# Kernel tuning notes

Hardware: AMD Instinct MI355X
Metric: run time of the kernel (lower is better)

The kernel has to match this reference:

```python
import jax, jax.numpy as jnp
import numpy as np

N, IN_C, HID, OUT_C = 4096, 512, 512, 40
E = 131072
N_CLUSTERS, PCA_K, KMEANS_ITERS = 7, 10, 10
EPS = 1e-12


def _linear_params(key, fin, fout):
    k1, k2 = jax.random.split(key)
    lim = 1.0 / np.sqrt(fin)
    W = jax.random.uniform(k1, (fin, fout), jnp.float32, -lim, lim)
    b = jax.random.uniform(k2, (fout,), jnp.float32, -lim, lim)
    return W, b


def setup_inputs() -> dict:
    key = jax.random.key(0)
    ks = jax.random.split(key, 8)
    x = jax.random.normal(ks[0], (N, IN_C), jnp.float32)
    edge_index = jax.random.randint(ks[1], (2, E), 0, N, dtype=jnp.int32)
    y = jax.random.randint(ks[2], (N,), 0, N_CLUSTERS, dtype=jnp.int32)
    W_ego, b_ego = _linear_params(ks[3], IN_C, HID)
    W_cos, b_cos = _linear_params(ks[4], IN_C, HID)
    W_glob, b_glob = _linear_params(ks[5], IN_C, HID)
    W_fc, b_fc = _linear_params(ks[6], HID + IN_C + HID + HID, OUT_C)
    return dict(x=x, W_ego=W_ego, b_ego=b_ego, W_cos=W_cos, b_cos=b_cos,
                W_glob=W_glob, b_glob=b_glob, W_fc=W_fc, b_fc=b_fc,
                edge_index=edge_index, y=y)


def _mp_layer(x, W, b, src, dst):
    # MessagePassingLayer: scatter-add lin(x)[src] at dst, then relu
    h = x @ W + b
    agg = jax.ops.segment_sum(h[src], dst, num_segments=N)
    return jax.nn.relu(agg)


def _dominant_mask(x):
    # Dominant branch: PCA(10) -> KMeans(n_clusters) -> keep nodes with dist <= median.
    # sklearn's randomized KMeans replaced by deterministic Lloyd iterations
    # (init = first N_CLUSTERS rows); whole pipeline is detached in the original.
    xs = jax.lax.stop_gradient(x)
    xc = xs - xs.mean(0, keepdims=True)
    _, _, vt = jnp.linalg.svd(xc, full_matrices=False)
    feats = xc @ vt[:PCA_K].T  # [N, PCA_K]

    def step(c, _):
        d2 = ((feats[:, None, :] - c[None]) ** 2).sum(-1)  # [N, K]
        lab = jnp.argmin(d2, axis=1)
        sums = jax.ops.segment_sum(feats, lab, num_segments=N_CLUSTERS)
        cnt = jax.ops.segment_sum(jnp.ones((N,), jnp.float32), lab, num_segments=N_CLUSTERS)
        newc = jnp.where(cnt[:, None] > 0, sums / jnp.maximum(cnt, 1.0)[:, None], c)
        return newc, None

    centers, _ = jax.lax.scan(step, feats[:N_CLUSTERS], None, length=KMEANS_ITERS)
    d2 = ((feats[:, None, :] - centers[None]) ** 2).sum(-1)
    lab = jnp.argmin(d2, axis=1)
    dist = jnp.linalg.norm(feats - centers[lab], axis=1)
    keep = dist <= jnp.median(dist)
    return jax.lax.stop_gradient(keep.astype(jnp.float32))


def _forward(x, W_ego, b_ego, W_cos, b_cos, W_glob, b_glob, W_fc, b_fc, src, dst):
    # --- ego branch: exact 2-hop (source_to_target) subgraph mean per node ---
    # B[i, j] = 1 iff edge j->i; subset(i) = {i} | 1-hop | 2-hop (set semantics via >0)
    B = jnp.zeros((N, N), jnp.float32).at[dst, src].add(1.0)
    reach = jnp.eye(N, dtype=jnp.float32) + B + B @ B
    Mf = (reach > 0).astype(jnp.float32)
    ego_feats = (Mf @ x) / Mf.sum(1, keepdims=True)

    # --- Dominant branch: zero out far-from-center nodes ---
    keep = _dominant_mask(x)
    cut_enc = x * keep[:, None]

    # --- cosine branch: segment softmax over outgoing edges grouped by src ---
    norm_x = x / jnp.maximum(jnp.linalg.norm(x, axis=1, keepdims=True), EPS)
    sims = (norm_x[src] * norm_x[dst]).sum(-1)  # [E]
    smax = jax.ops.segment_max(sims, src, num_segments=N)
    ex = jnp.exp(sims - smax[src])
    den = jax.ops.segment_sum(ex, src, num_segments=N)
    w = ex / jnp.maximum(den, EPS)[src]
    num = jax.ops.segment_sum(w[:, None] * x[dst], src, num_segments=N)
    wsum = jax.ops.segment_sum(w, src, num_segments=N)
    deg = jax.ops.segment_sum(jnp.ones((E,), jnp.float32), src, num_segments=N)
    cos_feats = jnp.where(deg[:, None] > 0, num / jnp.maximum(wsum, EPS)[:, None], x)

    # --- encoders + head ---
    global_feats = x @ W_glob + b_glob
    ego_enc = _mp_layer(ego_feats, W_ego, b_ego, src, dst)
    cosine_enc = _mp_layer(cos_feats, W_cos, b_cos, src, dst)
    combined = jnp.concatenate([ego_enc, cut_enc, cosine_enc, global_feats], axis=-1)
    return jax.nn.log_softmax(combined @ W_fc + b_fc, axis=1)


def reference(x, W_ego, b_ego, W_cos, b_cos, W_glob, b_glob, W_fc, b_fc, edge_index, y):
    src, dst = edge_index[0], edge_index[1]
    return _forward(x, W_ego, b_ego, W_cos, b_cos, W_glob, b_glob, W_fc, b_fc, src, dst)
```

## Files before the change

### kernel.cpp

```cpp
#include <hip/hip_runtime.h>
#include <math.h>

#define NN 4096
#define NC 512
#define NE 131072
#define KM_BLOCKS 16

typedef __bf16 bf16x8 __attribute__((ext_vector_type(8)));
typedef float f32x4 __attribute__((ext_vector_type(4)));
typedef unsigned short u16x8 __attribute__((ext_vector_type(8)));

__device__ __forceinline__ unsigned short f2b(float f){
  unsigned u = __float_as_uint(f);
  u += 0x7fffu + ((u >> 16) & 1u);
  return (unsigned short)(u >> 16);
}
__device__ __forceinline__ float b2f(unsigned short h){
  return __uint_as_float(((unsigned)h) << 16);
}
__device__ __forceinline__ float wredsum(float v){
  #pragma unroll
  for (int o = 32; o; o >>= 1) v += __shfl_xor(v, o, 64);
  return v;
}
__device__ __forceinline__ float wredmax(float v){
  #pragma unroll
  for (int o = 32; o; o >>= 1) v = fmaxf(v, __shfl_xor(v, o, 64));
  return v;
}

__global__ __launch_bounds__(256) void k_transconv(const float* __restrict__ src, int R, int C,
    unsigned short* __restrict__ dstT, int ldT, unsigned short* __restrict__ dstD){
  __shared__ unsigned short tile[64][65];
  int bc = blockIdx.x * 64, br = blockIdx.y * 64;
  int t = threadIdx.x, lc = t & 63, lr4 = t >> 6;
  for (int j = 0; j < 16; ++j){
    int r = br + lr4*16 + j, c = bc + lc;
    float v = (r < R && c < C) ? src[(size_t)r*C + c] : 0.f;
    unsigned short b = f2b(v);
    tile[lr4*16+j][lc] = b;
    if (dstD && r < R && c < C) dstD[(size_t)r*C + c] = b;
  }
  __syncthreads();
  for (int j = 0; j < 16; ++j){
    int cc = bc + lr4*16 + j, rr = br + lc;
    if (cc < C && rr < R) dstT[(size_t)cc*ldT + rr] = tile[lc][lr4*16+j];
  }
}

__global__ __launch_bounds__(256) void k_normx(const float* __restrict__ x, unsigned short* __restrict__ nx){
  int wid = threadIdx.x >> 6, lane = threadIdx.x & 63;
  int row = blockIdx.x*4 + wid;
  const float* xr = x + (size_t)row*NC + lane*8;
  float v[8]; float ss = 0.f;
  #pragma unroll
  for (int j=0;j<8;j++){ v[j] = xr[j]; ss += v[j]*v[j]; }
  ss = wredsum(ss);
  float sc = 1.0f / fmaxf(sqrtf(ss), 1e-12f);
  u16x8 o;
  #pragma unroll
  for (int j=0;j<8;j++) o[j] = f2b(v[j]*sc);
  *(u16x8*)(nx + (size_t)row*NC + lane*8) = o;
}

__global__ void k_count_b1(const int* __restrict__ src, const int* __restrict__ dst,
    int* cin, int* cout, unsigned long long* B1){
  int e = blockIdx.x*256 + threadIdx.x;
  if (e < NE){
    int s = src[e], d = dst[e];
    atomicAdd(&cout[s], 1);
    atomicAdd(&cin[d], 1);
    atomicOr(&B1[(size_t)d*64 + (s>>6)], 1ull << (s & 63));
  }
}
__global__ __launch_bounds__(1024) void k_scan(const int* __restrict__ cnt0, const int* __restrict__ cnt1,
    int* off0, int* off1, int* fill0, int* fill1){
  __shared__ int s[1024];
  int t = threadIdx.x;
  for (int arr = 0; arr < 2; ++arr){
    const int* cnt = arr ? cnt1 : cnt0;
    int* off = arr ? off1 : off0;
    int* fill = arr ? fill1 : fill0;
    int a0 = cnt[t*4], a1 = cnt[t*4+1], a2 = cnt[t*4+2], a3 = cnt[t*4+3];
    int ts = a0+a1+a2+a3;
    s[t] = ts; __syncthreads();
    for (int o = 1; o < 1024; o <<= 1){
      int v = (t >= o) ? s[t-o] : 0; __syncthreads();
      s[t] += v; __syncthreads();
    }
    int ex = s[t] - ts;
    off[t*4] = ex; off[t*4+1] = ex+a0; off[t*4+2] = ex+a0+a1; off[t*4+3] = ex+a0+a1+a2;
    fill[t*4] = ex; fill[t*4+1] = ex+a0; fill[t*4+2] = ex+a0+a1; fill[t*4+3] = ex+a0+a1+a2;
    if (t == 1023) off[4096] = s[1023];
    __syncthreads();
  }
}
__global__ void k_fill(const int* __restrict__ src, const int* __restrict__ dst,
    int* fin, int* fout, int* csr_in, int* csr_out){
  int e = blockIdx.x*256 + threadIdx.x;
// ... 103 lines not shown

__global__ __launch_bounds__(256) void k_cos(const unsigned short* __restrict__ nx,
    const unsigned short* __restrict__ xb,
    const int* __restrict__ off_out, const int* __restrict__ csr_out,
    unsigned short* __restrict__ cosf){
  __shared__ float simsb[4][256];
  int wid = threadIdx.x >> 6, lane = threadIdx.x & 63;
  int node = blockIdx.x*4 + wid;
  float own[8];
  { u16x8 o = *(const u16x8*)(nx + (size_t)node*NC + lane*8);
    #pragma unroll
    for (int j=0;j<8;j++) own[j] = b2f(o[j]); }
  int beg = off_out[node], end = off_out[node+1], deg = end - beg;
  float m = -3.0e38f;
  for (int e = 0; e < deg; ++e){
    int d = csr_out[beg+e];
    u16x8 nb = *(const u16x8*)(nx + (size_t)d*NC + lane*8);
    float sp = 0.f;
    #pragma unroll
    for (int j=0;j<8;j++) sp += own[j]*b2f(nb[j]);
    float s = wredsum(sp);
    if (e < 256 && lane == 0) simsb[wid][e] = s;
    m = fmaxf(m, s);
  }
  float den = 0.f, acc[8] = {0,0,0,0,0,0,0,0};
  for (int e = 0; e < deg; ++e){
    int d = csr_out[beg+e];
    float s;
    if (e < 256) s = simsb[wid][e];
    else {
      u16x8 nb = *(const u16x8*)(nx + (size_t)d*NC + lane*8);
      float sp = 0.f;
      #pragma unroll
      for (int j=0;j<8;j++) sp += own[j]*b2f(nb[j]);
      s = wredsum(sp);
    }
    float w = expf(s - m);
    den += w;
    u16x8 xv = *(const u16x8*)(xb + (size_t)d*NC + lane*8);
    #pragma unroll
    for (int j=0;j<8;j++) acc[j] += w * b2f(xv[j]);
  }
  u16x8 o;
  if (deg > 0){
    float r = 1.0f/den;
    #pragma unroll
    for (int j=0;j<8;j++) o[j] = f2b(acc[j]*r);
  } else {
    o = *(const u16x8*)(xb + (size_t)node*NC + lane*8);
  }
  *(u16x8*)(cosf + (size_t)node*NC + lane*8) = o;
}

__global__ __launch_bounds__(256) void k_agg(const unsigned short* __restrict__ he,
    const unsigned short* __restrict__ hc,
    const int* __restrict__ off_in, const int* __restrict__ csr_in,
    unsigned short* __restrict__ comb){
  int wid = threadIdx.x >> 6, lane = threadIdx.x & 63;
  int node = blockIdx.x*4 + wid;
  float ae[8] = {0,0,0,0,0,0,0,0}, ac[8] = {0,0,0,0,0,0,0,0};
  int beg = off_in[node], end = off_in[node+1];
  for (int e = beg; e < end; ++e){
    int j = csr_in[e];
    u16x8 ve = *(const u16x8*)(he + (size_t)j*NC + lane*8);
    u16x8 vc = *(const u16x8*)(hc + (size_t)j*NC + lane*8);
    #pragma unroll
    for (int k=0;k<8;k++){ ae[k] += b2f(ve[k]); ac[k] += b2f(vc[k]); }
  }
  u16x8 oe, oc;
  #pragma unroll
  for (int k=0;k<8;k++){ oe[k] = f2b(fmaxf(ae[k], 0.f)); oc[k] = f2b(fmaxf(ac[k], 0.f)); }
  *(u16x8*)(comb + (size_t)node*2048 + lane*8) = oe;
  *(u16x8*)(comb + (size_t)node*2048 + 1024 + lane*8) = oc;
}

__global__ void k_cut(const unsigned short* __restrict__ xb, const float* __restrict__ keep,
    unsigned short* __restrict__ comb){
  int id = blockIdx.x*256 + threadIdx.x;
  int node = id >> 6, lane = id & 63;
  u16x8 xv = *(const u16x8*)(xb + (size_t)node*NC + lane*8);
  if (keep[node] == 0.f){
    #pragma unroll
    for (int j=0;j<8;j++) xv[j] = 0;
  }
  *(u16x8*)(comb + (size_t)node*2048 + 512 + lane*8) = xv;
}

__global__ __launch_bounds__(256) void k_lsm(const float* __restrict__ logits, float* __restrict__ out){
  int wid = threadIdx.x >> 6, lane = threadIdx.x & 63;
  int row = blockIdx.x*4 + wid;
  float v = (lane < 40) ? logits[(size_t)row*64 + lane] : -3.0e38f;
  float m = wredmax(v);
  float e = (lane < 40) ? expf(v - m) : 0.f;
  float s = wredsum(e);
  float l = logf(s);
  if (lane < 40) out[(size_t)row*40 + lane] = v - m - l;
}

__global__ void k_colmean(const float* __restrict__ x, double* __restrict__ meanbuf){
  int c0 = threadIdx.x;
  int r0 = blockIdx.x*128;
  double s0 = 0, s1 = 0;
  for (int r = r0; r < r0+128; ++r){
    s0 += (double)x[(size_t)r*NC + c0];
    s1 += (double)x[(size_t)r*NC + c0 + 256];
  }
  atomicAdd(&meanbuf[c0], s0);
  atomicAdd(&meanbuf[c0+256], s1);
}

__global__ __launch_bounds__(256) void k_cov(const float* __restrict__ x,
    const double* __restrict__ meanbuf, double* __restrict__ Cm){
  __shared__ float sa[16][33];
  __shared__ float sb[16][33];
  const int t = threadIdx.x;
  const int ti = t & 15, tj = t >> 4;
  const int bi = blockIdx.x, bj = blockIdx.y;
  int l0 = t, l1 = t + 256;
  int r0a = l0 >> 5, c0a = l0 & 31;
  int r1a = l1 >> 5, c1a = l1 & 31;
  float ma0 = (float)(meanbuf[bi*32 + c0a] * (1.0/4096.0));
  float ma1 = (float)(meanbuf[bi*32 + c1a] * (1.0/4096.0));
  float mb0 = (float)(meanbuf[bj*32 + c0a] * (1.0/4096.0));
  float mb1 = (float)(meanbuf[bj*32 + c1a] * (1.0/4096.0));
  double a00=0,a01=0,a10=0,a11=0;
  for (int r0 = 0; r0 < NN; r0 += 16){
    sa[r0a][c0a] = x[(size_t)(r0 + r0a)*NC + bi*32 + c0a] - ma0;
    sa[r1a][c1a] = x[(size_t)(r0 + r1a)*NC + bi*32 + c1a] - ma1;
    sb[r0a][c0a] = x[(size_t)(r0 + r0a)*NC + bj*32 + c0a] - mb0;
    sb[r1a][c1a] = x[(size_t)(r0 + r1a)*NC + bj*32 + c1a] - mb1;
    __syncthreads();
    #pragma unroll
    for (int rr = 0; rr < 16; ++rr){
      double av0 = (double)sa[rr][ti], av1 = (double)sa[rr][ti+16];
      double bv0 = (double)sb[rr][tj], bv1 = (double)sb[rr][tj+16];
      a00 += av0*bv0; a01 += av0*bv1; a10 += av1*bv0; a11 += av1*bv1;
    }
    __syncthreads();
  }
  Cm[(size_t)(bi*32+ti)*512 + bj*32+tj]       = a00;
  Cm[(size_t)(bi*32+ti)*512 + bj*32+tj+16]    = a01;
  Cm[(size_t)(bi*32+ti+16)*512 + bj*32+tj]    = a10;
  Cm[(size_t)(bi*32+ti+16)*512 + bj*32+tj+16] = a11;
}

__global__ __launch_bounds__(256) void k_mm64(const double* __restrict__ A,
    const double* __restrict__ B, double* __restrict__ C){
  __shared__ double sa[32][17];
  __shared__ double sb[16][33];
  const int t = threadIdx.x;
  const int ti = t & 15, tj = t >> 4;
  const int bi = blockIdx.x, bj = blockIdx.y;
  double a00=0,a01=0,a10=0,a11=0;
  for (int k0 = 0; k0 < 512; k0 += 16){
    { int ii = t >> 4, kk = t & 15;
      sa[ii][kk] = A[(size_t)(bi*32+ii)*512 + k0+kk];
      int ii2 = (t+256) >> 4, kk2 = (t+256) & 15;
      sa[ii2][kk2] = A[(size_t)(bi*32+ii2)*512 + k0+kk2];
      int kk3 = t >> 5, jj3 = t & 31;
      sb[kk3][jj3] = B[(size_t)(k0+kk3)*512 + bj*32+jj3];
      int kk4 = (t+256) >> 5, jj4 = (t+256) & 31;
      sb[kk4][jj4] = B[(size_t)(k0+kk4)*512 + bj*32+jj4];
    }
    __syncthreads();
    #pragma unroll
    for (int kk = 0; kk < 16; ++kk){
      double av0 = sa[ti][kk], av1 = sa[ti+16][kk];
      double bv0 = sb[kk][tj], bv1 = sb[kk][tj+16];
      a00 += av0*bv0; a01 += av0*bv1; a10 += av1*bv0; a11 += av1*bv1;
    }
    __syncthreads();
  }
  C[(size_t)(bi*32+ti)*512 + bj*32+tj]       = a00;
  C[(size_t)(bi*32+ti)*512 + bj*32+tj+16]    = a01;
  C[(size_t)(bi*32+ti+16)*512 + bj*32+tj]    = a10;
  C[(size_t)(bi*32+ti+16)*512 + bj*32+tj+16] = a11;
}

__global__ __launch_bounds__(512) void k_diagmax2(const double* __restrict__ A,
    const double* __restrict__ B, double* __restrict__ scal){
  __shared__ double red[512];
  int t = threadIdx.x;
  for (int w = 0; w < 2; ++w){
    const double* M = w ? B : A;
    red[t] = M[(size_t)t*512 + t];
    __syncthreads();
    for (int o = 256; o; o >>= 1){ if (t < o) red[t] = fmax(red[t], red[t+o]); __syncthreads(); }
    if (t == 0) scal[w] = 1.0 / fmax(red[0], 1e-300);
    __syncthreads();
  }
}

__global__ void k_initV0(double* __restrict__ V){
  int id = blockIdx.x*256 + threadIdx.x;
  if (id < 16384){
    unsigned h = (unsigned)id * 2654435761u + 12345u;
    h ^= h >> 13; h *= 2246822519u; h ^= h >> 16;
    V[id] = ((double)(h & 0xffffu) / 32768.0) - 1.0;
  }
}

__global__ __launch_bounds__(256) void k_matV(const double* __restrict__ M,
    const double* __restrict__ Vin, double* __restrict__ Vout, const double* __restrict__ scal){
  int id = blockIdx.x*256 + threadIdx.x;
  int r = id >> 5, c = id & 31;
  const double* Mr = M + (size_t)r*512;
  double s0=0,s1=0,s2=0,s3=0;
  for (int k = 0; k < 512; k += 4){
    s0 += Mr[k]   * Vin[(size_t)k*32 + c];
    s1 += Mr[k+1] * Vin[(size_t)(k+1)*32 + c];
    s2 += Mr[k+2] * Vin[(size_t)(k+2)*32 + c];
    s3 += Mr[k+3] * Vin[(size_t)(k+3)*32 + c];
  }
  double s = (s0+s1)+(s2+s3);
  Vout[id] = scal ? s*scal[0] : s;
}

__global__ __launch_bounds__(1024) void k_G(const double* __restrict__ V,
    const double* __restrict__ Y, double* __restrict__ G){
  int t = threadIdx.x;
  int i = t >> 5, j = t & 31;
  double s = 0;
  for (int k = 0; k < 512; ++k) s += V[(size_t)k*32+i]*Y[(size_t)k*32+j];
  G[i*32+j] = s;
}

__global__ __launch_bounds__(1024) void k_gram_cholqr(double* __restrict__ V){
  __shared__ double L[32][33];
  int t = threadIdx.x;
  int i = t >> 5, j = t & 31;
  { double s = 0;
    for (int k = 0; k < 512; ++k) s += V[(size_t)k*32+i]*V[(size_t)k*32+j];
    L[i][j] = s; }
  __syncthreads();
  for (int k = 0; k < 32; ++k){
    if (t == 0) L[k][k] = sqrt(fmax(L[k][k], 1e-300));
    __syncthreads();
    if (t > k && t < 32) L[t][k] /= L[k][k];
    __syncthreads();
    if (i > k && j > k && j <= i) L[i][j] -= L[i][k]*L[j][k];
    __syncthreads();
  }
  if (t < 512){
    int r = t;
    double v[32];
    #pragma unroll
    for (int jj = 0; jj < 32; ++jj) v[jj] = V[(size_t)r*32 + jj];
    #pragma unroll
    for (int jj = 0; jj < 32; ++jj){
      double s = v[jj];
      #pragma unroll
      for (int ii = 0; ii < 32; ++ii) if (ii < jj) s -= L[jj][ii]*v[ii];
      v[jj] = s / L[jj][jj];
    }
    #pragma unroll
    for (int jj = 0; jj < 32; ++jj) V[(size_t)r*32 + jj] = v[jj];
  }
}

__global__ __launch_bounds__(256) void k_jacobi(const double* __restrict__ Gg,
    const double* __restrict__ Vg, float* __restrict__ P){
  __shared__ double G[32][33], H[32][33], Q[32][33];
  __shared__ double pcs[16], pss[16];
  __shared__ int pp[16], pq[16], map[32], idx[10];
  __shared__ double eig[32];
  int t = threadIdx.x;
  for (int l = t; l < 1024; l += 256){
    int i = l >> 5, j = l & 31;
    G[i][j] = 0.5*(Gg[i*32+j] + Gg[j*32+i]);
    Q[i][j] = (i == j) ? 1.0 : 0.0;
  }
  __syncthreads();
  for (int sweep = 0; sweep < 6; ++sweep)
  for (int r = 0; r < 31; ++r){
    if (t < 16){
      int u = (t == 0) ? 0 : ((r + t - 1) % 31) + 1;
      int v = ((r + 30 - t) % 31) + 1;
      int p_ = u < v ? u : v, q_ = u < v ? v : u;
      double app = G[p_][p_], aqq = G[q_][q_], apq = G[p_][q_];
      double c, s;
      if (fabs(apq) < 1e-280){ c = 1.0; s = 0.0; }
      else {
        double tau = (aqq - app)/(2.0*apq);
        double tt = (tau >= 0 ? 1.0 : -1.0)/(fabs(tau) + sqrt(1.0 + tau*tau));
        c = 1.0/sqrt(1.0 + tt*tt); s = tt*c;
      }
      pcs[t] = c; pss[t] = s; pp[t] = p_; pq[t] = q_;
      map[p_] = t; map[q_] = t | 32;
    }
    __syncthreads();
    for (int l = t; l < 1024; l += 256){
      int i = l >> 5, j = l & 31;
      int mi = map[i], k = mi & 31;
      double c = pcs[k], s = pss[k];
      double gp = G[pp[k]][j], gq = G[pq[k]][j];
      H[i][j] = (mi & 32) ? (s*gp + c*gq) : (c*gp - s*gq);
    }
    __syncthreads();
    for (int l = t; l < 512; l += 256){
      int i = l >> 4, k = l & 15;
      double c = pcs[k], s = pss[k];
      int p_ = pp[k], q_ = pq[k];
      double hp = H[i][p_], hq = H[i][q_];
      G[i][p_] = c*hp - s*hq; G[i][q_] = s*hp + c*hq;
      double qp = Q[i][p_], qq = Q[i][q_];
      Q[i][p_] = c*qp - s*qq; Q[i][q_] = s*qp + c*qq;
    }
    __syncthreads();
  }
  if (t == 0){
    for (int i2 = 0; i2 < 32; ++i2) eig[i2] = G[i2][i2];
    unsigned used = 0;
    for (int k = 0; k < 10; ++k){
      int best = 0; double bv = -1e300;
      for (int i2 = 0; i2 < 32; ++i2)
        if (!((used >> i2) & 1u) && eig[i2] > bv){ bv = eig[i2]; best = i2; }
      used |= 1u << best; idx[k] = best;
    }
  }
  __syncthreads();
  for (int l = t; l < 5120; l += 256){
    int k = l/10, j = l%10;
    int c = idx[j];
    double s2 = 0;
    for (int m = 0; m < 32; ++m) s2 += Vg[(size_t)k*32+m]*Q[m][c];
    P[k*10+j] = (float)s2;
  }
}

__global__ __launch_bounds__(256) void k_feats(const float* __restrict__ x,
    const double* __restrict__ meanbuf, const float* __restrict__ P,
    float* __restrict__ feats, float* __restrict__ cent){
  int id = blockIdx.x*256 + threadIdx.x;
  int n = id >> 4, j = id & 15;
  if (j < 10){
    float s = 0;
    for (int c = 0; c < 512; ++c)
      s += (x[(size_t)n*512+c] - (float)(meanbuf[c]*(1.0/4096.0))) * P[c*10+j];
    feats[n*10+j] = s;
    if (n < 7) cent[n*10+j] = s;
  }
}

__global__ __launch_bounds__(256) void k_assign(const float* __restrict__ feats,
    const float* __restrict__ cent, float* __restrict__ part){
  __shared__ float fs[256][10];
  __shared__ float cs[7][10];
  __shared__ unsigned char labs[256];
  int t = threadIdx.x, b = blockIdx.x;
  int base = b*256;
  if (t < 70) cs[t/10][t%10] = cent[t];
  for (int i = t; i < 2560; i += 256) fs[i/10][i%10] = feats[base*10 + i];
  __syncthreads();
  { float f[10];
    #pragma unroll
    for (int d = 0; d < 10; ++d) f[d] = fs[t][d];
    int best = 0; float bd = 3.0e38f;
    for (int k = 0; k < 7; ++k){
      float s = 0;
      #pragma unroll
      for (int d = 0; d < 10; ++d){ float df = f[d]-cs[k][d]; s += df*df; }
      if (s < bd){ bd = s; best = k; }
    }
    labs[t] = (unsigned char)best; }
  __syncthreads();
  if (t < 77){
    float acc = 0;
    if (t < 70){
      int k = t/10, d = t%10;
      for (int nn = 0; nn < 256; ++nn) if (labs[nn] == k) acc += fs[nn][d];
    } else {
      int k = t - 70;
      for (int nn = 0; nn < 256; ++nn) if (labs[nn] == k) acc += 1.f;
    }
    part[b*77 + t] = acc;
  }
}

__global__ __launch_bounds__(128) void k_newcent(const float* __restrict__ part, float* __restrict__ cent){
  __shared__ float sums[77];
  int t = threadIdx.x;
  if (t < 77){
    float s = 0;
    for (int b = 0; b < KM_BLOCKS; ++b) s += part[b*77 + t];
    sums[t] = s;
  }
  __syncthreads();
  if (t < 70){
    float cnt = sums[70 + t/10];
    if (cnt > 0.f) cent[t] = sums[t] / fmaxf(cnt, 1.f);
  }
}

__global__ __launch_bounds__(256) void k_dist(const float* __restrict__ feats,
    const float* __restrict__ cent, float* __restrict__ distb){
  __shared__ float cs[7][10];
  int t = threadIdx.x, n = blockIdx.x*256 + t;
  if (t < 70) cs[t/10][t%10] = cent[t];
  __syncthreads();
  float f[10];
  #pragma unroll
  for (int d = 0; d < 10; ++d) f[d] = feats[n*10 + d];
  float bd = 3.0e38f;
  for (int k = 0; k < 7; ++k){
    float s = 0;
    #pragma unroll
    for (int d = 0; d < 10; ++d){ float df = f[d]-cs[k][d]; s += df*df; }
    bd = fminf(bd, s);
  }
  distb[n] = sqrtf(bd);
}

__global__ __launch_bounds__(256) void k_median(const float* __restrict__ distb, float* __restrict__ keep){
  __shared__ unsigned u[4096];
  __shared__ int redc[4];
  int t = threadIdx.x;
  for (int i = t; i < 4096; i += 256) u[i] = __float_as_uint(distb[i]);
  __syncthreads();
  unsigned vals[2];
  for (int ri = 0; ri < 2; ++ri){
    int r = 2047 + ri;
    unsigned prefix = 0;
    for (int bit = 31; bit >= 0; --bit){
      unsigned hm = (bit < 31) ? (0xffffffffu << (bit+1)) : 0u;
      int c = 0;
      for (int i = t; i < 4096; i += 256){
        unsigned e = u[i];
        if ((e & hm) == prefix && !((e >> bit) & 1u)) c++;
      }
      #pragma unroll
      for (int o = 32; o; o >>= 1) c += __shfl_xor(c, o, 64);
      if ((t & 63) == 0) redc[t >> 6] = c;
      __syncthreads();
      int tot = redc[0] + redc[1] + redc[2] + redc[3];
      if (r >= tot){ prefix |= (1u << bit); r -= tot; }
      __syncthreads();
    }
    vals[ri] = prefix;
  }
  float med = 0.5f*(__uint_as_float(vals[0]) + __uint_as_float(vals[1]));
  for (int i = t; i < 4096; i += 256) keep[i] = (distb[i] <= med) ? 1.f : 0.f;
}

extern "C" void kernel_launch(void* const* d_in, const int* in_sizes, int n_in,
                              void* d_out, int out_size, void* d_ws, size_t ws_size,
                              hipStream_t stream){
  const float* x      = (const float*)d_in[0];
  const float* W_ego  = (const float*)d_in[1];
  const float* b_ego  = (const float*)d_in[2];
  const float* W_cos  = (const float*)d_in[3];
  const float* b_cos  = (const float*)d_in[4];
  const float* W_glob = (const float*)d_in[5];
  const float* b_glob = (const float*)d_in[6];
  const float* W_fc   = (const float*)d_in[7];
  const float* b_fc   = (const float*)d_in[8];
  const int*   ei     = (const int*)d_in[9];
  const int* src = ei;
  const int* dst = ei + NE;
  float* out = (float*)d_out;

  char* p = (char*)d_ws;
  auto alloc = [&](size_t n) -> char* { char* r = p; p += (n + 255) & ~(size_t)255; return r; };

  unsigned long long* B1 = (unsigned long long*)alloc((size_t)NN*64*8);
  unsigned short* Mf     = (unsigned short*)alloc((size_t)NN*NN*2);
  unsigned short* x_bf   = (unsigned short*)alloc((size_t)NN*NC*2);
  unsigned short* xT_bf  = (unsigned short*)alloc((size_t)NN*NC*2);
  unsigned short* nx_bf  = (unsigned short*)alloc((size_t)NN*NC*2);
  unsigned short* egof   = (unsigned short*)alloc((size_t)NN*NC*2);
  unsigned short* cosf   = (unsigned short*)alloc((size_t)NN*NC*2);
  unsigned short* h_ego  = (unsigned short*)alloc((size_t)NN*NC*2);
  unsigned short* h_cos  = (unsigned short*)alloc((size_t)NN*NC*2);
  unsigned short* WegoT  = (unsigned short*)alloc((size_t)512*512*2);
  unsigned short* WcosT  = (unsigned short*)alloc((size_t)512*512*2);
  unsigned short* WglobT = (unsigned short*)alloc((size_t)512*512*2);
  unsigned short* WfcT   = (unsigned short*)alloc((size_t)128*2048*2);
  unsigned short* comb   = (unsigned short*)alloc((size_t)NN*2048*2);
  float* logits   = (float*)alloc((size_t)NN*64*4);
  float* rowrecip = (float*)alloc((size_t)NN*4);
  float* keep     = (float*)alloc((size_t)NN*4);
  int* cnt_in   = (int*)alloc((size_t)NN*4);
  int* cnt_out  = (int*)alloc((size_t)NN*4);
  int* off_in   = (int*)alloc((size_t)(NN+1)*4);
  int* off_out  = (int*)alloc((size_t)(NN+1)*4);
  int* fill_in  = (int*)alloc((size_t)NN*4);
  int* fill_out = (int*)alloc((size_t)NN*4);
  int* csr_in   = (int*)alloc((size_t)NE*4);
  int* csr_out  = (int*)alloc((size_t)NE*4);
  double* meanbuf = (double*)alloc(512*8);
  double* Cm  = (double*)alloc((size_t)512*512*8);
  double* C2m = (double*)alloc((size_t)512*512*8);
  double* C4m = (double*)alloc((size_t)512*512*8);
  double* C8m = (double*)alloc((size_t)512*512*8);
  double* C16m = (double*)alloc((size_t)512*512*8);
  double* C32m = (double*)alloc((size_t)512*512*8);
  double* C64m = (double*)alloc((size_t)512*512*8);
  double* Va  = (double*)alloc((size_t)512*32*8);
  double* Vb  = (double*)alloc((size_t)512*32*8);
  double* Yb  = (double*)alloc((size_t)512*32*8);
  double* Gm  = (double*)alloc(32*32*8);
  double* scal = (double*)alloc(64);
  float* Pm    = (float*)alloc((size_t)512*10*4);
  float* feats = (float*)alloc((size_t)NN*10*4);
  float* cent  = (float*)alloc(128*4);
  float* part  = (float*)alloc((size_t)KM_BLOCKS*77*4);
  float* distb = (float*)alloc((size_t)NN*4);

  hipMemsetAsync(B1, 0, (size_t)NN*64*8, stream);
  hipMemsetAsync(cnt_in, 0, (size_t)NN*4, stream);
  hipMemsetAsync(cnt_out, 0, (size_t)NN*4, stream);
  hipMemsetAsync(meanbuf, 0, 512*8, stream);
  hipMemsetAsync(WfcT, 0, (size_t)128*2048*2, stream);

  k_transconv<<<dim3(8,64), 256, 0, stream>>>(x, NN, NC, xT_bf, NN, x_bf);
  k_transconv<<<dim3(8,8), 256, 0, stream>>>(W_ego, 512, 512, WegoT, 512, (unsigned short*)0);
  k_transconv<<<dim3(8,8), 256, 0, stream>>>(W_cos, 512, 512, WcosT, 512, (unsigned short*)0);
  k_transconv<<<dim3(8,8), 256, 0, stream>>>(W_glob, 512, 512, WglobT, 512, (unsigned short*)0);
  k_transconv<<<dim3(1,32), 256, 0, stream>>>(W_fc, 2048, 40, WfcT, 2048, (unsigned short*)0);
  k_normx<<<1024, 256, 0, stream>>>(x, nx_bf);

  k_count_b1<<<512, 256, 0, stream>>>(src, dst, cnt_in, cnt_out, B1);
  k_scan<<<1, 1024, 0, stream>>>(cnt_in, cnt_out, off_in, off_out, fill_in, fill_out);
  k_fill<<<512, 256, 0, stream>>>(src, dst, fill_in, fill_out, csr_in, csr_out);
  k_bits2<<<1024, 256, 0, stream>>>(B1, off_in, csr_in, Mf, rowrecip);

  gemm_bt<0><<<dim3(64,4), 256, 0, stream>>>(Mf, NN, xT_bf, NN, NN, NC,
      (float*)0, egof, NC, (const float*)0, rowrecip);

  k_colmean<<<32, 256, 0, stream>>>(x, meanbuf);
  k_cov<<<dim3(16,16), 256, 0, stream>>>(x, meanbuf, Cm);
  k_mm64<<<dim3(16,16), 256, 0, stream>>>(Cm,  Cm,  C2m);
  k_mm64<<<dim3(16,16), 256, 0, stream>>>(C2m, C2m, C4m);
  k_mm64<<<dim3(16,16), 256, 0, stream>>>(C4m, C4m, C8m);
  k_mm64<<<dim3(16,16), 256, 0, stream>>>(C8m, C8m, C16m);
  k_mm64<<<dim3(16,16), 256, 0, stream>>>(C16m, C16m, C32m);
  k_mm64<<<dim3(16,16), 256, 0, stream>>>(C32m, C32m, C64m);
  k_diagmax2<<<1, 512, 0, stream>>>(C16m, C64m, scal);
  k_initV0<<<64, 256, 0, stream>>>(Va);
  for (int it = 0; it < 2; ++it){
    k_matV<<<64, 256, 0, stream>>>(C64m, Va, Vb, scal + 1);
    k_matV<<<64, 256, 0, stream>>>(C16m, Vb, Va, scal + 0);
    k_gram_cholqr<<<1, 1024, 0, stream>>>(Va);
  }
  k_matV<<<64, 256, 0, stream>>>(Cm, Va, Yb, (const double*)0);
  k_G<<<1, 1024, 0, stream>>>(Va, Yb, Gm);
  k_jacobi<<<1, 256, 0, stream>>>(Gm, Va, Pm);
  k_feats<<<256, 256, 0, stream>>>(x, meanbuf, Pm, feats, cent);

  for (int it = 0; it < 10; ++it){
    k_assign<<<KM_BLOCKS, 256, 0, stream>>>(feats, cent, part);
    k_newcent<<<1, 128, 0, stream>>>(part, cent);
  }
  k_dist<<<KM_BLOCKS, 256, 0, stream>>>(feats, cent, distb);
  k_median<<<1, 256, 0, stream>>>(distb, keep);

  k_cos<<<1024, 256, 0, stream>>>(nx_bf, x_bf, off_out, csr_out, cosf);

  gemm_bt<1><<<dim3(64,4), 256, 0, stream>>>(egof, NC, WegoT, 512, 512, NC,
      (float*)0, h_ego, NC, b_ego, (const float*)0);
  gemm_bt<1><<<dim3(64,4), 256, 0, stream>>>(cosf, NC, WcosT, 512, 512, NC,
      (float*)0, h_cos, NC, b_cos, (const float*)0);
  gemm_bt<1><<<dim3(64,4), 256, 0, stream>>>(x_bf, NC, WglobT, 512, 512, NC,
      (float*)0, comb + 1536, 2048, b_glob, (const float*)0);

  k_agg<<<1024, 256, 0, stream>>>(h_ego, h_cos, off_in, csr_in, comb);
  k_cut<<<1024, 256, 0, stream>>>(x_bf, keep, comb);

  gemm_bt<2><<<dim3(64,1), 256, 0, stream>>>(comb, 2048, WfcT, 2048, 2048, 40,
      logits, (unsigned short*)0, 64, b_fc, (const float*)0);
  k_lsm<<<1024, 256, 0, stream>>>(logits, out);
}
```

Before: 1.932 ms.

## Fuse PCA/KMeans/median tail into one cooperative persistent kernel

Replaces about 35 small sequential launches (diagmax, subspace iteration matV/cholQR, Gram, Jacobi, feats, 10 KMeans assign/update rounds, dist, median) with one cooperative kernel of 64 blocks that uses grid-wide syncs. Each block keeps the centroids in shared memory and recomputes the reduction of partial sums redundantly, so the single-block centroid-update kernel is no longer needed. It also merges the three weight transposes into one launch and the agg and cut kernels into one. The aim is to remove launch overhead and serialization on tiny kernels. In exchange, the Cholesky now runs on 256 threads instead of 1024, so it does more work per thread, and the grid syncs add their own cost.

```diff
diff --git a/kernel.cpp b/kernel.cpp
--- a/kernel.cpp
+++ b/kernel.cpp
@@ -1,10 +1,12 @@
 #include <hip/hip_runtime.h>
+#include <hip/hip_cooperative_groups.h>
 #include <math.h>
+
+namespace cg = cooperative_groups;
 
 #define NN 4096
 #define NC 512
 #define NE 131072
-#define KM_BLOCKS 16
 
 typedef __bf16 bf16x8 __attribute__((ext_vector_type(8)));
 typedef float f32x4 __attribute__((ext_vector_type(4)));
@@ -45,6 +47,25 @@
   for (int j = 0; j < 16; ++j){
     int cc = bc + lr4*16 + j, rr = br + lc;
     if (cc < C && rr < R) dstT[(size_t)cc*ldT + rr] = tile[lc][lr4*16+j];
+  }
+}
+
+__global__ __launch_bounds__(256) void k_transconv3(const float* __restrict__ A,
+    const float* __restrict__ B, const float* __restrict__ C,
+    unsigned short* __restrict__ TA, unsigned short* __restrict__ TB, unsigned short* __restrict__ TC){
+  __shared__ unsigned short tile[64][65];
+  const float* src = (blockIdx.z == 0) ? A : ((blockIdx.z == 1) ? B : C);
+  unsigned short* dstT = (blockIdx.z == 0) ? TA : ((blockIdx.z == 1) ? TB : TC);
+  int bc = blockIdx.x * 64, br = blockIdx.y * 64;
+  int t = threadIdx.x, lc = t & 63, lr4 = t >> 6;
+  for (int j = 0; j < 16; ++j){
+    int r = br + lr4*16 + j, c = bc + lc;
+    tile[lr4*16+j][lc] = f2b(src[(size_t)r*512 + c]);
+  }
+  __syncthreads();
+  for (int j = 0; j < 16; ++j){
+    int cc = bc + lr4*16 + j, rr = br + lc;
+    dstT[(size_t)cc*512 + rr] = tile[lc][lr4*16+j];
   }
 }
 
@@ -254,9 +275,10 @@
   *(u16x8*)(cosf + (size_t)node*NC + lane*8) = o;
 }
 
-__global__ __launch_bounds__(256) void k_agg(const unsigned short* __restrict__ he,
+__global__ __launch_bounds__(256) void k_aggcut(const unsigned short* __restrict__ he,
     const unsigned short* __restrict__ hc,
     const int* __restrict__ off_in, const int* __restrict__ csr_in,
+    const unsigned short* __restrict__ xb, const float* __restrict__ keep,
     unsigned short* __restrict__ comb){
   int wid = threadIdx.x >> 6, lane = threadIdx.x & 63;
   int node = blockIdx.x*4 + wid;
@@ -274,12 +296,6 @@
   for (int k=0;k<8;k++){ oe[k] = f2b(fmaxf(ae[k], 0.f)); oc[k] = f2b(fmaxf(ac[k], 0.f)); }
   *(u16x8*)(comb + (size_t)node*2048 + lane*8) = oe;
   *(u16x8*)(comb + (size_t)node*2048 + 1024 + lane*8) = oc;
-}
-
-__global__ void k_cut(const unsigned short* __restrict__ xb, const float* __restrict__ keep,
-    unsigned short* __restrict__ comb){
-  int id = blockIdx.x*256 + threadIdx.x;
-  int node = id >> 6, lane = id & 63;
   u16x8 xv = *(const u16x8*)(xb + (size_t)node*NC + lane*8);
   if (keep[node] == 0.f){
     #pragma unroll
@@ -379,33 +395,30 @@
   C[(size_t)(bi*32+ti+16)*512 + bj*32+tj+16] = a11;
 }
 
-__global__ __launch_bounds__(512) void k_diagmax2(const double* __restrict__ A,
-    const double* __restrict__ B, double* __restrict__ scal){
-  __shared__ double red[512];
-  int t = threadIdx.x;
-  for (int w = 0; w < 2; ++w){
-    const double* M = w ? B : A;
-    red[t] = M[(size_t)t*512 + t];
-    __syncthreads();
-    for (int o = 256; o; o >>= 1){ if (t < o) red[t] = fmax(red[t], red[t+o]); __syncthreads(); }
-    if (t == 0) scal[w] = 1.0 / fmax(red[0], 1e-300);
-    __syncthreads();
-  }
-}
-
-__global__ void k_initV0(double* __restrict__ V){
-  int id = blockIdx.x*256 + threadIdx.x;
-  if (id < 16384){
-    unsigned h = (unsigned)id * 2654435761u + 12345u;
-    h ^= h >> 13; h *= 2246822519u; h ^= h >> 16;
-    V[id] = ((double)(h & 0xffffu) / 32768.0) - 1.0;
-  }
-}
-
-__global__ __launch_bounds__(256) void k_matV(const double* __restrict__ M,
-    const double* __restrict__ Vin, double* __restrict__ Vout, const double* __restrict__ scal){
-  int id = blockIdx.x*256 + threadIdx.x;
-  int r = id >> 5, c = id & 31;
+union TailSmem {
+  double red[256];
+  double L[32][33];
+  struct {
+    double G[32][33], H[32][33], Q[32][33];
+    double pcs[16], pss[16];
+    int pp[16], pq[16], map[32], idx[10];
+    double eig[32];
+  } jac;
+  struct {
+    float cs[7][10];
+    float fs[256][10];
+    unsigned char labs[256];
+    float sums[77];
+  } km;
+  struct {
+    unsigned u[4096];
+    int redc[4];
+  } med;
+};
+
+__device__ __forceinline__ void matv_step(const double* __restrict__ M,
+    const double* __restrict__ Vin, double* __restrict__ Vout, double scale, int gid){
+  int r = gid >> 5, c = gid & 31;
   const double* Mr = M + (size_t)r*512;
   double s0=0,s1=0,s2=0,s3=0;
   for (int k = 0; k < 512; k += 4){
@@ -414,234 +427,266 @@
     s2 += Mr[k+2] * Vin[(size_t)(k+2)*32 + c];
     s3 += Mr[k+3] * Vin[(size_t)(k+3)*32 + c];
   }
-  double s = (s0+s1)+(s2+s3);
-  Vout[id] = scal ? s*scal[0] : s;
-}
-
-__global__ __launch_bounds__(1024) void k_G(const double* __restrict__ V,
-    const double* __restrict__ Y, double* __restrict__ G){
-  int t = threadIdx.x;
-  int i = t >> 5, j = t & 31;
-  double s = 0;
-  for (int k = 0; k < 512; ++k) s += V[(size_t)k*32+i]*Y[(size_t)k*32+j];
-  G[i*32+j] = s;
-}
-
-__global__ __launch_bounds__(1024) void k_gram_cholqr(double* __restrict__ V){
-  __shared__ double L[32][33];
-  int t = threadIdx.x;
-  int i = t >> 5, j = t & 31;
-  { double s = 0;
-    for (int k = 0; k < 512; ++k) s += V[(size_t)k*32+i]*V[(size_t)k*32+j];
-    L[i][j] = s; }
-  __syncthreads();
-  for (int k = 0; k < 32; ++k){
-    if (t == 0) L[k][k] = sqrt(fmax(L[k][k], 1e-300));
-    __syncthreads();
-    if (t > k && t < 32) L[t][k] /= L[k][k];
-    __syncthreads();
-    if (i > k && j > k && j <= i) L[i][j] -= L[i][k]*L[j][k];
-    __syncthreads();
-  }
-  if (t < 512){
-    int r = t;
-    double v[32];
-    #pragma unroll
-    for (int jj = 0; jj < 32; ++jj) v[jj] = V[(size_t)r*32 + jj];
-    #pragma unroll
-    for (int jj = 0; jj < 32; ++jj){
-      double s = v[jj];
-      #pragma unroll
-      for (int ii = 0; ii < 32; ++ii) if (ii < jj) s -= L[jj][ii]*v[ii];
-      v[jj] = s / L[jj][jj];
-    }
-    #pragma unroll
-    for (int jj = 0; jj < 32; ++jj) V[(size_t)r*32 + jj] = v[jj];
-  }
-}
-
-__global__ __launch_bounds__(256) void k_jacobi(const double* __restrict__ Gg,
-    const double* __restrict__ Vg, float* __restrict__ P){
-  __shared__ double G[32][33], H[32][33], Q[32][33];
-  __shared__ double pcs[16], pss[16];
-  __shared__ int pp[16], pq[16], map[32], idx[10];
-  __shared__ double eig[32];
-  int t = threadIdx.x;
-  for (int l = t; l < 1024; l += 256){
-    int i = l >> 5, j = l & 31;
-    G[i][j] = 0.5*(Gg[i*32+j] + Gg[j*32+i]);
-    Q[i][j] = (i == j) ? 1.0 : 0.0;
-  }
-  __syncthreads();
-  for (int sweep = 0; sweep < 6; ++sweep)
-  for (int r = 0; r < 31; ++r){
+  Vout[gid] = ((s0+s1)+(s2+s3))*scale;
+}
+
+__global__ __launch_bounds__(256) void k_tail(
+    const double* __restrict__ Cm, const double* __restrict__ C16m, const double* __restrict__ C64m,
+    double* __restrict__ Va, double* __restrict__ Vb, double* __restrict__ Yb, double* __restrict__ Gm,
+    const float* __restrict__ x, const double* __restrict__ meanbuf, float* __restrict__ Pm,
+    float* __restrict__ feats, float* __restrict__ part2, float* __restrict__ distb,
+    float* __restrict__ keep){
+  cg::grid_group grid = cg::this_grid();
+  __shared__ TailSmem sm;
+  __shared__ double s_scal0, s_scal1;
+  const int t = threadIdx.x;
+  const int b = blockIdx.x;
+  const int gid = b*256 + t;
+
+  {
+    double m0 = -1e300, m1 = -1e300;
+    for (int i = t; i < 512; i += 256){
+      m0 = fmax(m0, C16m[(size_t)i*512 + i]);
+      m1 = fmax(m1, C64m[(size_t)i*512 + i]);
+    }
+    sm.red[t] = m0; __syncthreads();
+    for (int o = 128; o; o >>= 1){ if (t < o) sm.red[t] = fmax(sm.red[t], sm.red[t+o]); __syncthreads(); }
+    if (t == 0) s_scal0 = 1.0 / fmax(sm.red[0], 1e-300);
+    __syncthreads();
+    sm.red[t] = m1; __syncthreads();
+    for (int o = 128; o; o >>= 1){ if (t < o) sm.red[t] = fmax(sm.red[t], sm.red[t+o]); __syncthreads(); }
+    if (t == 0) s_scal1 = 1.0 / fmax(sm.red[0], 1e-300);
+    __syncthreads();
+  }
+
+  {
+    unsigned h = (unsigned)gid * 2654435761u + 12345u;
+    h ^= h >> 13; h *= 2246822519u; h ^= h >> 16;
+    Va[gid] = ((double)(h & 0xffffu) / 32768.0) - 1.0;
+  }
+  grid.sync();
+
+  for (int it = 0; it < 2; ++it){
+    matv_step(C64m, Va, Vb, s_scal1, gid);
+    grid.sync();
+    matv_step(C16m, Vb, Va, s_scal0, gid);
+    grid.sync();
     if (t < 16){
-      int u = (t == 0) ? 0 : ((r + t - 1) % 31) + 1;
-      int v = ((r + 30 - t) % 31) + 1;
-      int p_ = u < v ? u : v, q_ = u < v ? v : u;
-      double app = G[p_][p_], aqq = G[q_][q_], apq = G[p_][q_];
-      double c, s;
-      if (fabs(apq) < 1e-280){ c = 1.0; s = 0.0; }
-      else {
-        double tau = (aqq - app)/(2.0*apq);
-        double tt = (tau >= 0 ? 1.0 : -1.0)/(fabs(tau) + sqrt(1.0 + tau*tau));
-        c = 1.0/sqrt(1.0 + tt*tt); s = tt*c;
-      }
-      pcs[t] = c; pss[t] = s; pp[t] = p_; pq[t] = q_;
-      map[p_] = t; map[q_] = t | 32;
-    }
-    __syncthreads();
+      int e = b*16 + t; int i = e >> 5, j = e & 31;
+      double s = 0;
+      for (int k = 0; k < 512; ++k) s += Va[(size_t)k*32+i]*Va[(size_t)k*32+j];
+      Gm[e] = s;
+    }
+    grid.sync();
+    {
+      for (int l = t; l < 1024; l += 256){ int i = l >> 5, j = l & 31; sm.L[i][j] = Gm[l]; }
+      __syncthreads();
+      for (int k = 0; k < 32; ++k){
+        if (t == 0) sm.L[k][k] = sqrt(fmax(sm.L[k][k], 1e-300));
+        __syncthreads();
+        if (t > k && t < 32) sm.L[t][k] /= sm.L[k][k];
+        __syncthreads();
+        for (int l = t; l < 1024; l += 256){
+          int i = l >> 5, j = l & 31;
+          if (i > k && j > k && j <= i) sm.L[i][j] -= sm.L[i][k]*sm.L[j][k];
+        }
+        __syncthreads();
+      }
+      if (t < 8){
+        int r = b*8 + t;
+        double v[32];
+        #pragma unroll
+        for (int jj = 0; jj < 32; ++jj) v[jj] = Va[(size_t)r*32 + jj];
+        #pragma unroll
+        for (int jj = 0; jj < 32; ++jj){
+          double s = v[jj];
+          #pragma unroll
+          for (int ii = 0; ii < 32; ++ii) if (ii < jj) s -= sm.L[jj][ii]*v[ii];
+          v[jj] = s / sm.L[jj][jj];
+        }
+        #pragma unroll
+        for (int jj = 0; jj < 32; ++jj) Va[(size_t)r*32 + jj] = v[jj];
+      }
+      __syncthreads();
+    }
+    grid.sync();
+  }
+
+  matv_step(Cm, Va, Yb, 1.0, gid);
+  grid.sync();
+
+  if (t < 16){
+    int e = b*16 + t; int i = e >> 5, j = e & 31;
+    double s = 0;
+    for (int k = 0; k < 512; ++k) s += Va[(size_t)k*32+i]*Yb[(size_t)k*32+j];
+    Gm[e] = s;
+  }
+  grid.sync();
+
+  if (b == 0){
     for (int l = t; l < 1024; l += 256){
       int i = l >> 5, j = l & 31;
-      int mi = map[i], k = mi & 31;
-      double c = pcs[k], s = pss[k];
-      double gp = G[pp[k]][j], gq = G[pq[k]][j];
-      H[i][j] = (mi & 32) ? (s*gp + c*gq) : (c*gp - s*gq);
-    }
-    __syncthreads();
-    for (int l = t; l < 512; l += 256){
-      int i = l >> 4, k = l & 15;
-      double c = pcs[k], s = pss[k];
-      int p_ = pp[k], q_ = pq[k];
-      double hp = H[i][p_], hq = H[i][q_];
-      G[i][p_] = c*hp - s*hq; G[i][q_] = s*hp + c*hq;
-      double qp = Q[i][p_], qq = Q[i][q_];
-      Q[i][p_] = c*qp - s*qq; Q[i][q_] = s*qp + c*qq;
-    }
-    __syncthreads();
-  }
-  if (t == 0){
-    for (int i2 = 0; i2 < 32; ++i2) eig[i2] = G[i2][i2];
-    unsigned used = 0;
-    for (int k = 0; k < 10; ++k){
-      int best = 0; double bv = -1e300;
-      for (int i2 = 0; i2 < 32; ++i2)
-        if (!((used >> i2) & 1u) && eig[i2] > bv){ bv = eig[i2]; best = i2; }
-      used |= 1u << best; idx[k] = best;
-    }
+      sm.jac.G[i][j] = 0.5*(Gm[i*32+j] + Gm[j*32+i]);
+      sm.jac.Q[i][j] = (i == j) ? 1.0 : 0.0;
+    }
+    __syncthreads();
+    for (int sweep = 0; sweep < 6; ++sweep)
+    for (int r = 0; r < 31; ++r){
+      if (t < 16){
+        int u = (t == 0) ? 0 : ((r + t - 1) % 31) + 1;
+        int v = ((r + 30 - t) % 31) + 1;
+        int p_ = u < v ? u : v, q_ = u < v ? v : u;
+        double app = sm.jac.G[p_][p_], aqq = sm.jac.G[q_][q_], apq = sm.jac.G[p_][q_];
+        double c, s;
+        if (fabs(apq) < 1e-280){ c = 1.0; s = 0.0; }
+        else {
+          double tau = (aqq - app)/(2.0*apq);
+          double tt = (tau >= 0 ? 1.0 : -1.0)/(fabs(tau) + sqrt(1.0 + tau*tau));
+          c = 1.0/sqrt(1.0 + tt*tt); s = tt*c;
+        }
+        sm.jac.pcs[t] = c; sm.jac.pss[t] = s; sm.jac.pp[t] = p_; sm.jac.pq[t] = q_;
+        sm.jac.map[p_] = t; sm.jac.map[q_] = t | 32;
+      }
+      __syncthreads();
+      for (int l = t; l < 1024; l += 256){
+        int i = l >> 5, j = l & 31;
+        int mi = sm.jac.map[i], k = mi & 31;
+        double c = sm.jac.pcs[k], s = sm.jac.pss[k];
+        double gp = sm.jac.G[sm.jac.pp[k]][j], gq = sm.jac.G[sm.jac.pq[k]][j];
+        sm.jac.H[i][j] = (mi & 32) ? (s*gp + c*gq) : (c*gp - s*gq);
+      }
+      __syncthreads();
+      for (int l = t; l < 512; l += 256){
+        int i = l >> 4, k = l & 15;
+        double c = sm.jac.pcs[k], s = sm.jac.pss[k];
+        int p_ = sm.jac.pp[k], q_ = sm.jac.pq[k];
+        double hp = sm.jac.H[i][p_], hq = sm.jac.H[i][q_];
+        sm.jac.G[i][p_] = c*hp - s*hq; sm.jac.G[i][q_] = s*hp + c*hq;
+        double qp = sm.jac.Q[i][p_], qq = sm.jac.Q[i][q_];
+        sm.jac.Q[i][p_] = c*qp - s*qq; sm.jac.Q[i][q_] = s*qp + c*qq;
+      }
+      __syncthreads();
+    }
+    if (t == 0){
+      for (int i2 = 0; i2 < 32; ++i2) sm.jac.eig[i2] = sm.jac.G[i2][i2];
+      unsigned used = 0;
+      for (int k = 0; k < 10; ++k){
+        int best = 0; double bv = -1e300;
+        for (int i2 = 0; i2 < 32; ++i2)
+          if (!((used >> i2) & 1u) && sm.jac.eig[i2] > bv){ bv = sm.jac.eig[i2]; best = i2; }
+        used |= 1u << best; sm.jac.idx[k] = best;
+      }
+    }
+    __syncthreads();
+    for (int l = t; l < 5120; l += 256){
+      int k = l/10, j = l%10;
+      int c = sm.jac.idx[j];
+      double s2 = 0;
+      for (int m = 0; m < 32; ++m) s2 += Va[(size_t)k*32+m]*sm.jac.Q[m][c];
+      Pm[k*10+j] = (float)s2;
+    }
+  }
+  grid.sync();
+
+  for (int id = gid; id < 65536; id += 16384){
+    int n = id >> 4, j = id & 15;
+    if (j < 10){
+      float s = 0;
+      for (int c2 = 0; c2 < 512; ++c2)
+        s += (x[(size_t)n*512+c2] - (float)(meanbuf[c2]*(1.0/4096.0))) * Pm[c2*10+j];
+      feats[n*10+j] = s;
+    }
+  }
+  grid.sync();
+
+  if (t < 70) sm.km.cs[t/10][t%10] = feats[t];
+  if (b < 16){
+    int base = b*256;
+    for (int i = t; i < 2560; i += 256) sm.km.fs[i/10][i%10] = feats[base*10 + i];
   }
   __syncthreads();
-  for (int l = t; l < 5120; l += 256){
-    int k = l/10, j = l%10;
-    int c = idx[j];
-    double s2 = 0;
-    for (int m = 0; m < 32; ++m) s2 += Vg[(size_t)k*32+m]*Q[m][c];
-    P[k*10+j] = (float)s2;
-  }
-}
-
-__global__ __launch_bounds__(256) void k_feats(const float* __restrict__ x,
-    const double* __restrict__ meanbuf, const float* __restrict__ P,
-    float* __restrict__ feats, float* __restrict__ cent){
-  int id = blockIdx.x*256 + threadIdx.x;
-  int n = id >> 4, j = id & 15;
-  if (j < 10){
-    float s = 0;
-    for (int c = 0; c < 512; ++c)
-      s += (x[(size_t)n*512+c] - (float)(meanbuf[c]*(1.0/4096.0))) * P[c*10+j];
-    feats[n*10+j] = s;
-    if (n < 7) cent[n*10+j] = s;
-  }
-}
-
-__global__ __launch_bounds__(256) void k_assign(const float* __restrict__ feats,
-    const float* __restrict__ cent, float* __restrict__ part){
-  __shared__ float fs[256][10];
-  __shared__ float cs[7][10];
-  __shared__ unsigned char labs[256];
-  int t = threadIdx.x, b = blockIdx.x;
-  int base = b*256;
-  if (t < 70) cs[t/10][t%10] = cent[t];
-  for (int i = t; i < 2560; i += 256) fs[i/10][i%10] = feats[base*10 + i];
-  __syncthreads();
-  { float f[10];
-    #pragma unroll
-    for (int d = 0; d < 10; ++d) f[d] = fs[t][d];
-    int best = 0; float bd = 3.0e38f;
+  for (int iter = 0; iter < 10; ++iter){
+    float* pbuf = part2 + (size_t)(iter & 1)*16*77;
+    if (b < 16){
+      float f[10];
+      #pragma unroll
+      for (int d = 0; d < 10; ++d) f[d] = sm.km.fs[t][d];
+      int best = 0; float bd = 3.0e38f;
+      for (int k = 0; k < 7; ++k){
+        float s = 0;
+        #pragma unroll
+        for (int d = 0; d < 10; ++d){ float df = f[d]-sm.km.cs[k][d]; s += df*df; }
+        if (s < bd){ bd = s; best = k; }
+      }
+      sm.km.labs[t] = (unsigned char)best;
+      __syncthreads();
+      if (t < 77){
+        float acc = 0;
+        if (t < 70){
+          int k = t/10, d = t%10;
+          for (int nn = 0; nn < 256; ++nn) if (sm.km.labs[nn] == k) acc += sm.km.fs[nn][d];
+        } else {
+          int k = t - 70;
+          for (int nn = 0; nn < 256; ++nn) if (sm.km.labs[nn] == k) acc += 1.f;
+        }
+        pbuf[b*77 + t] = acc;
+      }
+    }
+    grid.sync();
+    if (t < 77){
+      float s = 0;
+      for (int bb = 0; bb < 16; ++bb) s += pbuf[bb*77 + t];
+      sm.km.sums[t] = s;
+    }
+    __syncthreads();
+    if (t < 70){
+      float cnt = sm.km.sums[70 + t/10];
+      if (cnt > 0.f) sm.km.cs[t/10][t%10] = sm.km.sums[t] / fmaxf(cnt, 1.f);
+    }
+    __syncthreads();
+  }
+  if (b < 16){
+    float f[10];
+    #pragma unroll
+    for (int d = 0; d < 10; ++d) f[d] = sm.km.fs[t][d];
+    float bd = 3.0e38f;
     for (int k = 0; k < 7; ++k){
       float s = 0;
       #pragma unroll
-      for (int d = 0; d < 10; ++d){ float df = f[d]-cs[k][d]; s += df*df; }
-      if (s < bd){ bd = s; best = k; }
-    }
-    labs[t] = (unsigned char)best; }
-  __syncthreads();
-  if (t < 77){
-    float acc = 0;
-    if (t < 70){
-      int k = t/10, d = t%10;
-      for (int nn = 0; nn < 256; ++nn) if (labs[nn] == k) acc += fs[nn][d];
-    } else {
-      int k = t - 70;
-      for (int nn = 0; nn < 256; ++nn) if (labs[nn] == k) acc += 1.f;
-    }
-    part[b*77 + t] = acc;
-  }
-}
-
-__global__ __launch_bounds__(128) void k_newcent(const float* __restrict__ part, float* __restrict__ cent){
-  __shared__ float sums[77];
-  int t = threadIdx.x;
-  if (t < 77){
-    float s = 0;
-    for (int b = 0; b < KM_BLOCKS; ++b) s += part[b*77 + t];
-    sums[t] = s;
-  }
-  __syncthreads();
-  if (t < 70){
-    float cnt = sums[70 + t/10];
-    if (cnt > 0.f) cent[t] = sums[t] / fmaxf(cnt, 1.f);
-  }
-}
-
-__global__ __launch_bounds__(256) void k_dist(const float* __restrict__ feats,
-    const float* __restrict__ cent, float* __restrict__ distb){
-  __shared__ float cs[7][10];
-  int t = threadIdx.x, n = blockIdx.x*256 + t;
-  if (t < 70) cs[t/10][t%10] = cent[t];
-  __syncthreads();
-  float f[10];
-  #pragma unroll
-  for (int d = 0; d < 10; ++d) f[d] = feats[n*10 + d];
-  float bd = 3.0e38f;
-  for (int k = 0; k < 7; ++k){
-    float s = 0;
-    #pragma unroll
-    for (int d = 0; d < 10; ++d){ float df = f[d]-cs[k][d]; s += df*df; }
-    bd = fminf(bd, s);
-  }
-  distb[n] = sqrtf(bd);
-}
-
-__global__ __launch_bounds__(256) void k_median(const float* __restrict__ distb, float* __restrict__ keep){
-  __shared__ unsigned u[4096];
-  __shared__ int redc[4];
-  int t = threadIdx.x;
-  for (int i = t; i < 4096; i += 256) u[i] = __float_as_uint(distb[i]);
-  __syncthreads();
-  unsigned vals[2];
-  for (int ri = 0; ri < 2; ++ri){
-    int r = 2047 + ri;
-    unsigned prefix = 0;
-    for (int bit = 31; bit >= 0; --bit){
-      unsigned hm = (bit < 31) ? (0xffffffffu << (bit+1)) : 0u;
-      int c = 0;
-      for (int i = t; i < 4096; i += 256){
-        unsigned e = u[i];
-        if ((e & hm) == prefix && !((e >> bit) & 1u)) c++;
-      }
-      #pragma unroll
-      for (int o = 32; o; o >>= 1) c += __shfl_xor(c, o, 64);
-      if ((t & 63) == 0) redc[t >> 6] = c;
-      __syncthreads();
-      int tot = redc[0] + redc[1] + redc[2] + redc[3];
-      if (r >= tot){ prefix |= (1u << bit); r -= tot; }
-      __syncthreads();
-    }
-    vals[ri] = prefix;
-  }
-  float med = 0.5f*(__uint_as_float(vals[0]) + __uint_as_float(vals[1]));
-  for (int i = t; i < 4096; i += 256) keep[i] = (distb[i] <= med) ? 1.f : 0.f;
+      for (int d = 0; d < 10; ++d){ float df = f[d]-sm.km.cs[k][d]; s += df*df; }
+      bd = fminf(bd, s);
+    }
+    distb[b*256 + t] = sqrtf(bd);
+  }
+  grid.sync();
+
+  if (b == 0){
+    for (int i = t; i < 4096; i += 256) sm.med.u[i] = __float_as_uint(distb[i]);
+    __syncthreads();
+    unsigned vals[2];
+    for (int ri = 0; ri < 2; ++ri){
+      int r = 2047 + ri;
+      unsigned prefix = 0;
+      for (int bit = 31; bit >= 0; --bit){
+        unsigned hm = (bit < 31) ? (0xffffffffu << (bit+1)) : 0u;
+        int c = 0;
+        for (int i = t; i < 4096; i += 256){
+          unsigned e = sm.med.u[i];
+          if ((e & hm) == prefix && !((e >> bit) & 1u)) c++;
+        }
+        #pragma unroll
+        for (int o = 32; o; o >>= 1) c += __shfl_xor(c, o, 64);
+        if ((t & 63) == 0) sm.med.redc[t >> 6] = c;
+        __syncthreads();
+        int tot = sm.med.redc[0] + sm.med.redc[1] + sm.med.redc[2] + sm.med.redc[3];
+        if (r >= tot){ prefix |= (1u << bit); r -= tot; }
+        __syncthreads();
+      }
+      vals[ri] = prefix;
+    }
+    float med = 0.5f*(__uint_as_float(vals[0]) + __uint_as_float(vals[1]));
+    for (int i = t; i < 4096; i += 256) keep[i] = (distb[i] <= med) ? 1.f : 0.f;
+  }
 }
 
 extern "C" void kernel_launch(void* const* d_in, const int* in_sizes, int n_in,
@@ -701,11 +746,9 @@
   double* Vb  = (double*)alloc((size_t)512*32*8);
   double* Yb  = (double*)alloc((size_t)512*32*8);
   double* Gm  = (double*)alloc(32*32*8);
-  double* scal = (double*)alloc(64);
   float* Pm    = (float*)alloc((size_t)512*10*4);
   float* feats = (float*)alloc((size_t)NN*10*4);
-  float* cent  = (float*)alloc(128*4);
-  float* part  = (float*)alloc((size_t)KM_BLOCKS*77*4);
+  float* part  = (float*)alloc((size_t)2*16*77*4);
   float* distb = (float*)alloc((size_t)NN*4);
 
   hipMemsetAsync(B1, 0, (size_t)NN*64*8, stream);
@@ -715,9 +758,7 @@
   hipMemsetAsync(WfcT, 0, (size_t)128*2048*2, stream);
 
   k_transconv<<<dim3(8,64), 256, 0, stream>>>(x, NN, NC, xT_bf, NN, x_bf);
-  k_transconv<<<dim3(8,8), 256, 0, stream>>>(W_ego, 512, 512, WegoT, 512, (unsigned short*)0);
-  k_transconv<<<dim3(8,8), 256, 0, stream>>>(W_cos, 512, 512, WcosT, 512, (unsigned short*)0);
-  k_transconv<<<dim3(8,8), 256, 0, stream>>>(W_glob, 512, 512, WglobT, 512, (unsigned short*)0);
+  k_transconv3<<<dim3(8,8,3), 256, 0, stream>>>(W_ego, W_cos, W_glob, WegoT, WcosT, WglobT);
   k_transconv<<<dim3(1,32), 256, 0, stream>>>(W_fc, 2048, 40, WfcT, 2048, (unsigned short*)0);
   k_normx<<<1024, 256, 0, stream>>>(x, nx_bf);
 
@@ -737,24 +778,13 @@
   k_mm64<<<dim3(16,16), 256, 0, stream>>>(C8m, C8m, C16m);
   k_mm64<<<dim3(16,16), 256, 0, stream>>>(C16m, C16m, C32m);
   k_mm64<<<dim3(16,16), 256, 0, stream>>>(C32m, C32m, C64m);
-  k_diagmax2<<<1, 512, 0, stream>>>(C16m, C64m, scal);
-  k_initV0<<<64, 256, 0, stream>>>(Va);
-  for (int it = 0; it < 2; ++it){
-    k_matV<<<64, 256, 0, stream>>>(C64m, Va, Vb, scal + 1);
-    k_matV<<<64, 256, 0, stream>>>(C16m, Vb, Va, scal + 0);
-    k_gram_cholqr<<<1, 1024, 0, stream>>>(Va);
-  }
-  k_matV<<<64, 256, 0, stream>>>(Cm, Va, Yb, (const double*)0);
-  k_G<<<1, 1024, 0, stream>>>(Va, Yb, Gm);
-  k_jacobi<<<1, 256, 0, stream>>>(Gm, Va, Pm);
-  k_feats<<<256, 256, 0, stream>>>(x, meanbuf, Pm, feats, cent);
-
-  for (int it = 0; it < 10; ++it){
-    k_assign<<<KM_BLOCKS, 256, 0, stream>>>(feats, cent, part);
-    k_newcent<<<1, 128, 0, stream>>>(part, cent);
-  }
-  k_dist<<<KM_BLOCKS, 256, 0, stream>>>(feats, cent, distb);
-  k_median<<<1, 256, 0, stream>>>(distb, keep);
+
+  {
+    void* args[] = { (void*)&Cm, (void*)&C16m, (void*)&C64m, (void*)&Va, (void*)&Vb,
+                     (void*)&Yb, (void*)&Gm, (void*)&x, (void*)&meanbuf, (void*)&Pm,
+                     (void*)&feats, (void*)&part, (void*)&distb, (void*)&keep };
+    hipLaunchCooperativeKernel((void*)k_tail, dim3(64), dim3(256), args, 0, stream);
+  }
 
   k_cos<<<1024, 256, 0, stream>>>(nx_bf, x_bf, off_out, csr_out, cosf);
 
@@ -765,8 +795,7 @@
   gemm_bt<1><<<dim3(64,4), 256, 0, stream>>>(x_bf, NC, WglobT, 512, 512, NC,
       (float*)0, comb + 1536, 2048, b_glob, (const float*)0);
 
-  k_agg<<<1024, 256, 0, stream>>>(h_ego, h_cos, off_in, csr_in, comb);
-  k_cut<<<1024, 256, 0, stream>>>(x_bf, keep, comb);
+  k_aggcut<<<1024, 256, 0, stream>>>(h_ego, h_cos, off_in, csr_in, x_bf, keep, comb);
 
   gemm_bt<2><<<dim3(64,1), 256, 0, stream>>>(comb, 2048, WfcT, 2048, 2048, 40,
       logits, (unsigned short*)0, 64, b_fc, (const float*)0);
```

After: 1.826 ms, median of 2. -5.5%, faster.
